# Kernel optimization log

Hardware: AMD Instinct MI355X
Metric: run time of the kernel (lower is better)

The kernel has to match this reference:

```python
import jax, jax.numpy as jnp
import numpy as np

HEAD_DIM = 64

def setup_inputs() -> dict:
    key = jax.random.key(0)
    k1, k2, k3, k4, k5 = jax.random.split(key, 5)
    T, B, E = 2048, 4, 1024
    KD = 64  # kdim
    x = jax.random.normal(k1, (T, B, E), dtype=jnp.float32)
    in_proj_weight = jax.random.normal(k2, (3 * KD, HEAD_DIM), dtype=jnp.float32) * (1.0 / np.sqrt(HEAD_DIM))
    in_proj_bias = jnp.zeros((3 * KD,), dtype=jnp.float32)
    out_w = jax.random.normal(k4, (HEAD_DIM, KD), dtype=jnp.float32) * (1.0 / np.sqrt(KD))
    out_b = jnp.zeros((HEAD_DIM,), dtype=jnp.float32)
    return {"x": x, "in_proj_weight": in_proj_weight, "in_proj_bias": in_proj_bias,
            "out_w": out_w, "out_b": out_b}

def reference(x, in_proj_weight, in_proj_bias, out_w, out_b):
    # x: [T, B, E] with E = H * HEAD_DIM (qkv_same self-attention path)
    T, B, E = x.shape
    H = E // HEAD_DIM
    KD = in_proj_weight.shape[0] // 3
    scaling = HEAD_DIM ** (-0.5)
    # reshape splits embed dim into heads: [T, B*H, 64]
    xh = x.reshape(T, B * H, HEAD_DIM)
    # fused in-projection: [T, B*H, 3*KD], then chunk into q/k/v
    qkv = xh @ in_proj_weight.T + in_proj_bias
    q, k, v = jnp.split(qkv, 3, axis=-1)          # each [T, B*H, KD]
    q = q * scaling
    q = q.transpose(1, 0, 2)                      # [B*H, T, KD]
    k = k.transpose(1, 0, 2)
    v = v.transpose(1, 0, 2)
    scores = jnp.einsum('btd,bsd->bts', q, k)     # [B*H, T, T]
    w = jax.nn.softmax(scores, axis=-1)
    attn = jnp.einsum('bts,bsd->btd', w, v)       # [B*H, T, KD]
    attn = attn.transpose(1, 0, 2).reshape(T, B, H, KD)
    out = attn @ out_w.T + out_b                  # [T, B, H, HEAD_DIM]
    out = out.reshape(T, B, H * HEAD_DIM)         # [T, B, E]
    # averaged attention weights over heads: [B, T, T]
    avg_w = w.reshape(B, H, T, T).sum(axis=1) / H
    return out, avg_w
```

## Files before the change

### kernel.cpp

```cpp
#include <hip/hip_runtime.h>
#include <hip/hip_bf16.h>

#define T_DIM 2048
#define B_DIM 4
#define E_DIM 1024

typedef __bf16 bf16_t;
typedef bf16_t bf16x8 __attribute__((ext_vector_type(8)));
typedef float f32x4 __attribute__((ext_vector_type(4)));
typedef float f32x16 __attribute__((ext_vector_type(16)));

union frag_u { uint4 u; bf16x8 b; };

constexpr float SCALEQ = 0.18033688011112042f;

__device__ __forceinline__ f32x16 mfma32(bf16x8 a, bf16x8 b, f32x16 c) {
  return __builtin_amdgcn_mfma_f32_32x32x16_bf16(a, b, c, 0, 0, 0);
}
__device__ __forceinline__ unsigned packbf(float a, float b) {
  union { bf16_t h[2]; unsigned u; } r;
  r.h[0] = (bf16_t)a; r.h[1] = (bf16_t)b; return r.u;
}
__device__ __forceinline__ void pl32swap(unsigned &x, unsigned &y) {
  asm volatile("v_permlane32_swap_b32 %0, %1" : "+v"(x), "+v"(y));
}
__device__ __forceinline__ void gload16(const void* g, void* l) {
  __builtin_amdgcn_global_load_lds((const __attribute__((address_space(1))) void*)g,
                                   (__attribute__((address_space(3))) void*)l, 16, 0, 0);
}
__device__ __forceinline__ bf16x8 ldc(const char* base, int chunk, int row) {
  frag_u f; f.u = *(const uint4*)(base + chunk * 1024 + row * 16); return f.b;
}
__device__ __forceinline__ float ex2(float x) { return __builtin_amdgcn_exp2f(x); }

#define VMCNT2 do { asm volatile("s_waitcnt vmcnt(2)" ::: "memory"); \
                    __builtin_amdgcn_sched_barrier(0); } while (0)
#define VMCNT0 do { asm volatile("s_waitcnt vmcnt(0)" ::: "memory"); \
                    __builtin_amdgcn_sched_barrier(0); } while (0)
#define LGKM0  do { asm volatile("s_waitcnt lgkmcnt(0)" ::: "memory"); \
                    __builtin_amdgcn_sched_barrier(0); } while (0)

template <int O>
__device__ __forceinline__ uint4 mkfrag(const f32x16& A) {
  unsigned X = packbf(A[O + 0], A[O + 1]);
  unsigned Z = packbf(A[O + 2], A[O + 3]);
  unsigned Y = packbf(A[O + 4], A[O + 5]);
  unsigned W = packbf(A[O + 6], A[O + 7]);
  pl32swap(X, Y); pl32swap(Z, W);
  return (uint4){X, Z, Y, W};
}

__global__ __launch_bounds__(256) void qkv_kernel(
    const float* __restrict__ x, const float* __restrict__ W,
    const float* __restrict__ bias,
    bf16_t* __restrict__ Qc, bf16_t* __restrict__ Kc, bf16_t* __restrict__ Vc) {
  __shared__ __align__(16) char xlds[16384];
  __shared__ __align__(16) char wlds[24576];
  __shared__ float bs[192];
  const int tid = threadIdx.x;
  const int bh = blockIdx.x >> 4;
  const int tt = blockIdx.x & 15;
  const int b = bh >> 4, h = bh & 15;
  const int t0 = tt * 128;
  const int wid = tid >> 6, lane = tid & 63;
  const int lq = lane & 31, hi = lane >> 5;

  for (int i = tid; i < 1024; i += 256) {
    int t = i >> 3, oct = i & 7;
    const float* src = x + ((size_t)(t0 + t) * B_DIM + b) * E_DIM + h * 64 + oct * 8;
    float4 f0 = *(const float4*)src;
    float4 f1 = *(const float4*)(src + 4);
    uint4 u;
    u.x = packbf(f0.x, f0.y); u.y = packbf(f0.z, f0.w);
    u.z = packbf(f1.x, f1.y); u.w = packbf(f1.z, f1.w);
    *(uint4*)(xlds + oct * 2048 + t * 16) = u;
  }
  for (int i = tid; i < 1536; i += 256) {
    int r = i >> 3, oct = i & 7;
    const float* src = W + r * 64 + oct * 8;
    float4 f0 = *(const float4*)src;
    float4 f1 = *(const float4*)(src + 4);
    uint4 u;
    u.x = packbf(f0.x, f0.y); u.y = packbf(f0.z, f0.w);
    u.z = packbf(f1.x, f1.y); u.w = packbf(f1.z, f1.w);
    *(uint4*)(wlds + oct * 3072 + r * 16) = u;
  }
  if (tid < 192) bs[tid] = bias[tid];
  __syncthreads();

  frag_u bx[4];
  #pragma unroll
  for (int s = 0; s < 4; ++s)
    bx[s].u = *(const uint4*)(xlds + (s * 2 + hi) * 2048 + (wid * 32 + lq) * 16);

  f32x16 acc[6];
  #pragma unroll
  for (int mt = 0; mt < 6; ++mt)
    #pragma unroll
    for (int r = 0; r < 16; ++r) acc[mt][r] = 0.f;

  #pragma unroll
  for (int mt = 0; mt < 6; ++mt) {
    #pragma unroll
    for (int s = 0; s < 4; ++s) {
      frag_u aw;
      aw.u = *(const uint4*)(wlds + (s * 2 + hi) * 3072 + (mt * 32 + lq) * 16);
      acc[mt] = mfma32(aw.b, bx[s].b, acc[mt]);
    }
  }

  const size_t tb = ((size_t)bh * 32 + (t0 >> 6) + (wid >> 1)) * 4096;
  const int trow = (wid & 1) * 32 + lq;

  #pragma unroll
  for (int mt = 0; mt < 6; ++mt) {
    #pragma unroll
    for (int g = 0; g < 4; ++g) {
      int rbase = mt * 32 + 8 * g + 4 * hi;
      float4 bq = *(const float4*)&bs[rbase];
      float v0 = acc[mt][4 * g + 0] + bq.x;
      float v1 = acc[mt][4 * g + 1] + bq.y;
      float v2 = acc[mt][4 * g + 2] + bq.z;
      float v3 = acc[mt][4 * g + 3] + bq.w;
      if (mt < 2) {
        union { ushort4 us; unsigned u2[2]; } pk;
        pk.u2[0] = packbf(v0 * SCALEQ, v1 * SCALEQ);
        pk.u2[1] = packbf(v2 * SCALEQ, v3 * SCALEQ);
        int d0 = rbase;
        *(ushort4*)(Qc + tb + (d0 >> 3) * 512 + trow * 8 + (d0 & 7)) = pk.us;
      } else if (mt < 4) {
        union { ushort4 us; unsigned u2[2]; } pk;
        pk.u2[0] = packbf(v0, v1);
        pk.u2[1] = packbf(v2, v3);
        int d0 = rbase - 64;
        *(ushort4*)(Kc + tb + (d0 >> 3) * 512 + trow * 8 + (d0 & 7)) = pk.us;
      } else {
        int d0 = rbase - 128;
        bf16_t* vdst = Vc + tb + (trow >> 3) * 512 + (trow & 7);
        vdst[(size_t)(d0 + 0) * 8] = (bf16_t)v0;
        vdst[(size_t)(d0 + 1) * 8] = (bf16_t)v1;
        vdst[(size_t)(d0 + 2) * 8] = (bf16_t)v2;
        vdst[(size_t)(d0 + 3) * 8] = (bf16_t)v3;
      }
    }
  }
}

__global__ __launch_bounds__(512, 2) void flash_kernel(
    const bf16_t* __restrict__ Qc, const bf16_t* __restrict__ Kc,
    const bf16_t* __restrict__ Vc,
    const float* __restrict__ Wo, const float* __restrict__ bo,
    float* __restrict__ out, float* __restrict__ Lv) {
  __shared__ __align__(16) char lds[32768];
  __shared__ __align__(16) char wlds[8192];
  const int tid = threadIdx.x;
  const int bid = ((blockIdx.x & 7) << 6) | (blockIdx.x >> 3);
  const int bh = bid >> 3, qb = bid & 7;
  const int b = bh >> 4, h = bh & 15;
  const int wid = tid >> 6, lane = tid & 63;
  const int lq = lane & 31, hi = lane >> 5;
  const int qw = qb * 256 + wid * 32;

  {
    const float* src = Wo + (tid >> 3) * 64 + (tid & 7) * 8;
    float4 f0 = *(const float4*)src;
    float4 f1 = *(const float4*)(src + 4);
    uint4 u;
    u.x = packbf(f0.x, f0.y); u.y = packbf(f0.z, f0.w);
    u.z = packbf(f1.x, f1.y); u.w = packbf(f1.z, f1.w);
    *(uint4*)(wlds + (tid & 7) * 1024 + (tid >> 3) * 16) = u;
  }

  const bf16_t* qtb = Qc + ((size_t)bh * 32 + (qw >> 6)) * 4096;
  const int qrow = qw & 63;
  frag_u qf[4];
  #pragma unroll
  for (int s = 0; s < 4; ++s)
    qf[s].u = *(const uint4*)(qtb + (s * 2 + hi) * 512 + (qrow + lq) * 8);

  f32x16 zc;
  #pragma unroll
  for (int i = 0; i < 16; ++i) zc[i] = 0.f;

  f32x16 o0, o1;
  #pragma unroll
  for (int i = 0; i < 16; ++i) { o0[i] = 0.f; o1[i] = 0.f; }
  float lacc = 0.f;

  const bf16_t* kbh = Kc + (size_t)bh * 131072;
  const bf16_t* vbh = Vc + (size_t)bh * 131072;
  auto stage = [&](int buf, int t) {
    char* kd = lds + buf * 16384;
    const bf16_t* kt = kbh + (size_t)t * 4096 + wid * 512 + lane * 8;
    const bf16_t* vt = vbh + (size_t)t * 4096 + wid * 512 + lane * 8;
    gload16(kt, kd + wid * 1024);
    gload16(vt, kd + 8192 + wid * 1024);
  };

  stage(0, 0); stage(1, 1);
  __syncthreads();

  for (int t = 0; t < 32; ++t) {
    const char* kl = lds + (t & 1) * 16384;
    const char* vl = kl + 8192;

    bf16x8 k0[4], k1[4];
    #pragma unroll
    for (int s = 0; s < 4; ++s) {
      k0[s] = ldc(kl, s * 2 + hi, lq);
      k1[s] = ldc(kl, s * 2 + hi, 32 + lq);
    }
    f32x16 a0, a1;
    __builtin_amdgcn_s_setprio(1);
    a0 = mfma32(k0[0], qf[0].b, zc);
    a1 = mfma32(k1[0], qf[0].b, zc);
    #pragma unroll
    for (int s = 1; s < 4; ++s) {
      a0 = mfma32(k0[s], qf[s].b, a0);
      a1 = mfma32(k1[s], qf[s].b, a1);
    }
    __builtin_amdgcn_s_setprio(0);

    bf16x8 v0[4], v1[4];
    #pragma unroll
    for (int ks = 0; ks < 4; ++ks) {
      v0[ks] = ldc(vl, ks * 2 + hi, lq);
      v1[ks] = ldc(vl, ks * 2 + hi, 32 + lq);
    }
    LGKM0;
    __builtin_amdgcn_s_barrier();
    if (t + 2 < 32) stage(t & 1, t + 2);

    float s0 = 0.f, s1 = 0.f;
    #pragma unroll
    for (int i = 0; i < 16; ++i) {
      a0[i] = ex2(a0[i]); s0 += a0[i];
      a1[i] = ex2(a1[i]); s1 += a1[i];
    }
    lacc += s0 + s1;

    frag_u p0, p1, p2, p3;
    p0.u = mkfrag<0>(a0); p1.u = mkfrag<8>(a0);
    p2.u = mkfrag<0>(a1); p3.u = mkfrag<8>(a1);

    __builtin_amdgcn_s_setprio(1);
    o0 = mfma32(v0[0], p0.b, o0); o1 = mfma32(v1[0], p0.b, o1);
    o0 = mfma32(v0[1], p1.b, o0); o1 = mfma32(v1[1], p1.b, o1);
    o0 = mfma32(v0[2], p2.b, o0); o1 = mfma32(v1[2], p2.b, o1);
    o0 = mfma32(v0[3], p3.b, o0); o1 = mfma32(v1[3], p3.b, o1);
    __builtin_amdgcn_s_setprio(0);

    if (t < 30) { VMCNT2; } else { VMCNT0; }
    __builtin_amdgcn_s_barrier();
  }

  float lt = lacc + __shfl_xor(lacc, 32);
  float inv = 1.f / lt;
  #pragma unroll
  for (int i = 0; i < 16; ++i) { o0[i] *= inv; o1[i] *= inv; }

  frag_u fo[4];
  fo[0].u = mkfrag<0>(o0); fo[1].u = mkfrag<8>(o0);
  fo[2].u = mkfrag<0>(o1); fo[3].u = mkfrag<8>(o1);

  f32x16 c0, c1;
  {
    frag_u w0, w1;
    w0.u = *(const uint4*)(wlds + (0 * 2 + hi) * 1024 + lq * 16);
    w1.u = *(const uint4*)(wlds + (0 * 2 + hi) * 1024 + (32 + lq) * 16);
    c0 = mfma32(fo[0].b, w0.b, zc);
    c1 = mfma32(fo[0].b, w1.b, zc);
    #pragma unroll
    for (int s = 1; s < 4; ++s) {
      w0.u = *(const uint4*)(wlds + (s * 2 + hi) * 1024 + lq * 16);
      w1.u = *(const uint4*)(wlds + (s * 2 + hi) * 1024 + (32 + lq) * 16);
      c0 = mfma32(fo[s].b, w0.b, c0);
      c1 = mfma32(fo[s].b, w1.b, c1);
    }
  }
  float bo0 = bo[lq], bo1 = bo[32 + lq];
  #pragma unroll
  for (int r = 0; r < 16; ++r) {
    int tr = qw + (r & 3) + 8 * (r >> 2) + 4 * hi;
    out[((size_t)tr * B_DIM + b) * E_DIM + h * 64 + lq]      = c0[r] + bo0;
    out[((size_t)tr * B_DIM + b) * E_DIM + h * 64 + 32 + lq] = c1[r] + bo1;
  }
  if (lane < 32)
    Lv[(size_t)bh * T_DIM + qw + lq] = lt;
}

__global__ __launch_bounds__(512, 2) void avgw_kernel(
    const bf16_t* __restrict__ Qc, const bf16_t* __restrict__ Kc,
    const float* __restrict__ Lv, float* __restrict__ avgw) {
  __shared__ __align__(16) char qlds[2][16384];
  __shared__ __align__(16) char klds[2][16384];
  __shared__ float lw[16][128];
  const int tid = threadIdx.x;
  const int bid = ((blockIdx.x & 7) << 7) | (blockIdx.x >> 3);
  const int b = bid >> 8, tq = (bid >> 4) & 15, sq = bid & 15;
  const int t0 = tq * 128, s0 = sq * 128;
  const int wid = tid >> 6, lane = tid & 63;
  const int lq = lane & 31, hi = lane >> 5;
  const int wr = wid >> 2, wc = wid & 3;

  for (int i = tid; i < 2048; i += 512) {
    int h = i >> 7, tt = i & 127;
    size_t idx = ((size_t)(b * 16 + h)) * T_DIM + t0 + tt;
    lw[h][tt] = 1.0f / (16.0f * Lv[idx]);
  }

  auto stage = [&](int buf, int h) {
    int bh = b * 16 + h;
    const bf16_t* qt = Qc + ((size_t)bh * 32 + (t0 >> 6)) * 4096;
    const bf16_t* kt = Kc + ((size_t)bh * 32 + (s0 >> 6)) * 4096;
    #pragma unroll
    for (int j = 0; j < 2; ++j) {
      gload16(qt + wid * 1024 + j * 512 + lane * 8, qlds[buf] + wid * 2048 + j * 1024);
      gload16(kt + wid * 1024 + j * 512 + lane * 8, klds[buf] + wid * 2048 + j * 1024);
    }
  };

  f32x16 zc;
  #pragma unroll
  for (int r = 0; r < 16; ++r) zc[r] = 0.f;

  f32x16 sacc[2];
  #pragma unroll
  for (int i = 0; i < 2; ++i)
    #pragma unroll
    for (int r = 0; r < 16; ++r) sacc[i][r] = 0.f;

  stage(0, 0);
  __syncthreads();

  for (int h = 0; h < 16; ++h) {
    if (h < 15) stage((h + 1) & 1, h + 1);
    const char* qb = qlds[h & 1];
    const char* kb = klds[h & 1];

    frag_u aq[2][4], ak[4];
    #pragma unroll
    for (int s = 0; s < 4; ++s) {
      int rk = wc * 32 + lq;
      ak[s].u = *(const uint4*)(kb + (rk >> 6) * 8192 + (s * 2 + hi) * 1024 + (rk & 63) * 16);
      #pragma unroll
      for (int i = 0; i < 2; ++i) {
        int rq = wr * 64 + i * 32 + lq;
        aq[i][s].u = *(const uint4*)(qb + (rq >> 6) * 8192 + (s * 2 + hi) * 1024 + (rq & 63) * 16);
      }
    }

    #pragma unroll
    for (int i = 0; i < 2; ++i) {
      __builtin_amdgcn_s_setprio(1);
      f32x16 c = mfma32(aq[i][0].b, ak[0].b, zc);
      #pragma unroll
      for (int s = 1; s < 4; ++s) c = mfma32(aq[i][s].b, ak[s].b, c);
      __builtin_amdgcn_s_setprio(0);
      #pragma unroll
      for (int g = 0; g < 4; ++g) {
        f32x4 l4 = *(const f32x4*)&lw[h][wr * 64 + i * 32 + 8 * g + 4 * hi];
        #pragma unroll
        for (int e = 0; e < 4; ++e)
          sacc[i][4 * g + e] += ex2(c[4 * g + e]) * l4[e];
      }
    }
    __syncthreads();
  }

  #pragma unroll
  for (int i = 0; i < 2; ++i)
    #pragma unroll
    for (int r = 0; r < 16; ++r) {
      int trow = t0 + wr * 64 + i * 32 + (r & 3) + ((r >> 2) << 3) + (hi << 2);
      int scol = s0 + wc * 32 + lq;
      avgw[((size_t)b * T_DIM + trow) * T_DIM + scol] = sacc[i][r];
    }
}

extern "C" void kernel_launch(void* const* d_in, const int* in_sizes, int n_in,
                              void* d_out, int out_size, void* d_ws, size_t ws_size,
                              hipStream_t stream) {
  const float* x    = (const float*)d_in[0];
  const float* W    = (const float*)d_in[1];
  const float* bias = (const float*)d_in[2];
  const float* Wo   = (const float*)d_in[3];
  const float* bo   = (const float*)d_in[4];
  float* out  = (float*)d_out;
  float* avgw = out + (size_t)T_DIM * B_DIM * E_DIM;

  char* ws = (char*)d_ws;
  bf16_t* Qc = (bf16_t*)(ws);
  bf16_t* Kc = (bf16_t*)(ws + (16u << 20));
  bf16_t* Vc = (bf16_t*)(ws + (32u << 20));
  float*  Lv = (float*)(ws + (48u << 20));

  qkv_kernel<<<dim3(1024), dim3(256), 0, stream>>>(x, W, bias, Qc, Kc, Vc);
  flash_kernel<<<dim3(512), dim3(512), 0, stream>>>(Qc, Kc, Vc, Wo, bo, out, Lv);
  avgw_kernel<<<dim3(1024), dim3(512), 0, stream>>>(Qc, Kc, Lv, avgw);
}
```

Before: 175.7 us.

## Halve flash block to 4 waves with two ping-ponged 32-row query tiles per wave

The flash kernel now runs 256 threads per block, and each wave owns 64 query rows split into two 32-row sub-tiles (A and B). Their QK^T MFMAs, exp2/softmax and PV MFMAs are staggered so vector work on one sub-tile overlaps matrix work on the other, and the next tile's QK for A is issued early. Each K/V tile is staged with twice as many loads per thread, and the wait scheme changes accordingly. The goal is to hide softmax latency and halve per-block K/V LDS reads per query, at the cost of more accumulator registers and fewer waves per CU.

```diff
diff --git a/kernel.cpp b/kernel.cpp
--- a/kernel.cpp
+++ b/kernel.cpp
@@ -33,11 +33,13 @@
 }
 __device__ __forceinline__ float ex2(float x) { return __builtin_amdgcn_exp2f(x); }
 
-#define VMCNT2 do { asm volatile("s_waitcnt vmcnt(2)" ::: "memory"); \
+#define VMCNT4 do { asm volatile("s_waitcnt vmcnt(4)" ::: "memory"); \
                     __builtin_amdgcn_sched_barrier(0); } while (0)
 #define VMCNT0 do { asm volatile("s_waitcnt vmcnt(0)" ::: "memory"); \
                     __builtin_amdgcn_sched_barrier(0); } while (0)
 #define LGKM0  do { asm volatile("s_waitcnt lgkmcnt(0)" ::: "memory"); \
+                    __builtin_amdgcn_sched_barrier(0); } while (0)
+#define SBAR   do { __builtin_amdgcn_s_barrier(); \
                     __builtin_amdgcn_sched_barrier(0); } while (0)
 
 template <int O>
@@ -146,7 +148,7 @@
   }
 }
 
-__global__ __launch_bounds__(512, 2) void flash_kernel(
+__global__ __launch_bounds__(256, 2) void flash_kernel(
     const bf16_t* __restrict__ Qc, const bf16_t* __restrict__ Kc,
     const bf16_t* __restrict__ Vc,
     const float* __restrict__ Wo, const float* __restrict__ bo,
@@ -159,67 +161,93 @@
   const int b = bh >> 4, h = bh & 15;
   const int wid = tid >> 6, lane = tid & 63;
   const int lq = lane & 31, hi = lane >> 5;
-  const int qw = qb * 256 + wid * 32;
-
-  {
-    const float* src = Wo + (tid >> 3) * 64 + (tid & 7) * 8;
+  const int qw = qb * 256 + wid * 64;
+
+  for (int i = tid; i < 512; i += 256) {
+    int d = i >> 3, oct = i & 7;
+    const float* src = Wo + d * 64 + oct * 8;
     float4 f0 = *(const float4*)src;
     float4 f1 = *(const float4*)(src + 4);
     uint4 u;
     u.x = packbf(f0.x, f0.y); u.y = packbf(f0.z, f0.w);
     u.z = packbf(f1.x, f1.y); u.w = packbf(f1.z, f1.w);
-    *(uint4*)(wlds + (tid & 7) * 1024 + (tid >> 3) * 16) = u;
+    *(uint4*)(wlds + oct * 1024 + d * 16) = u;
   }
 
   const bf16_t* qtb = Qc + ((size_t)bh * 32 + (qw >> 6)) * 4096;
-  const int qrow = qw & 63;
-  frag_u qf[4];
-  #pragma unroll
-  for (int s = 0; s < 4; ++s)
-    qf[s].u = *(const uint4*)(qtb + (s * 2 + hi) * 512 + (qrow + lq) * 8);
+  frag_u qfA[4], qfB[4];
+  #pragma unroll
+  for (int s = 0; s < 4; ++s) {
+    qfA[s].u = *(const uint4*)(qtb + (s * 2 + hi) * 512 + lq * 8);
+    qfB[s].u = *(const uint4*)(qtb + (s * 2 + hi) * 512 + (32 + lq) * 8);
+  }
 
   f32x16 zc;
   #pragma unroll
   for (int i = 0; i < 16; ++i) zc[i] = 0.f;
 
-  f32x16 o0, o1;
-  #pragma unroll
-  for (int i = 0; i < 16; ++i) { o0[i] = 0.f; o1[i] = 0.f; }
-  float lacc = 0.f;
+  f32x16 oA0, oA1, oB0, oB1;
+  #pragma unroll
+  for (int i = 0; i < 16; ++i) { oA0[i] = 0.f; oA1[i] = 0.f; oB0[i] = 0.f; oB1[i] = 0.f; }
+  float lAacc = 0.f, lBacc = 0.f;
 
   const bf16_t* kbh = Kc + (size_t)bh * 131072;
   const bf16_t* vbh = Vc + (size_t)bh * 131072;
   auto stage = [&](int buf, int t) {
-    char* kd = lds + buf * 16384;
+    char* kl_ = lds + buf * 16384 + wid * 1024;
+    char* vl_ = kl_ + 8192;
     const bf16_t* kt = kbh + (size_t)t * 4096 + wid * 512 + lane * 8;
     const bf16_t* vt = vbh + (size_t)t * 4096 + wid * 512 + lane * 8;
-    gload16(kt, kd + wid * 1024);
-    gload16(vt, kd + 8192 + wid * 1024);
+    gload16(kt, kl_); gload16(kt + 2048, kl_ + 4096);
+    gload16(vt, vl_); gload16(vt + 2048, vl_ + 4096);
   };
 
   stage(0, 0); stage(1, 1);
-  __syncthreads();
-
-  for (int t = 0; t < 32; ++t) {
-    const char* kl = lds + (t & 1) * 16384;
-    const char* vl = kl + 8192;
-
-    bf16x8 k0[4], k1[4];
+  VMCNT4; LGKM0;
+  SBAR;
+
+  bf16x8 k0[4], k1[4];
+  {
+    const char* kl = lds;
     #pragma unroll
     for (int s = 0; s < 4; ++s) {
       k0[s] = ldc(kl, s * 2 + hi, lq);
       k1[s] = ldc(kl, s * 2 + hi, 32 + lq);
     }
-    f32x16 a0, a1;
+  }
+  f32x16 aA0, aA1;
+  aA0 = mfma32(k0[0], qfA[0].b, zc);
+  aA1 = mfma32(k1[0], qfA[0].b, zc);
+  #pragma unroll
+  for (int s = 1; s < 4; ++s) {
+    aA0 = mfma32(k0[s], qfA[s].b, aA0);
+    aA1 = mfma32(k1[s], qfA[s].b, aA1);
+  }
+
+  for (int t = 0; t < 32; ++t) {
+    const char* cb = lds + (t & 1) * 16384;
+    const char* vl = cb + 8192;
+
+    f32x16 aB0, aB1;
     __builtin_amdgcn_s_setprio(1);
-    a0 = mfma32(k0[0], qf[0].b, zc);
-    a1 = mfma32(k1[0], qf[0].b, zc);
+    aB0 = mfma32(k0[0], qfB[0].b, zc);
+    aB1 = mfma32(k1[0], qfB[0].b, zc);
     #pragma unroll
     for (int s = 1; s < 4; ++s) {
-      a0 = mfma32(k0[s], qf[s].b, a0);
-      a1 = mfma32(k1[s], qf[s].b, a1);
+      aB0 = mfma32(k0[s], qfB[s].b, aB0);
+      aB1 = mfma32(k1[s], qfB[s].b, aB1);
     }
     __builtin_amdgcn_s_setprio(0);
+    float sA = 0.f;
+    #pragma unroll
+    for (int i = 0; i < 16; ++i) {
+      aA0[i] = ex2(aA0[i]); sA += aA0[i];
+      aA1[i] = ex2(aA1[i]); sA += aA1[i];
+    }
+    lAacc += sA;
+    frag_u pA0, pA1, pA2, pA3;
+    pA0.u = mkfrag<0>(aA0); pA1.u = mkfrag<8>(aA0);
+    pA2.u = mkfrag<0>(aA1); pA3.u = mkfrag<8>(aA1);
 
     bf16x8 v0[4], v1[4];
     #pragma unroll
@@ -227,66 +255,92 @@
       v0[ks] = ldc(vl, ks * 2 + hi, lq);
       v1[ks] = ldc(vl, ks * 2 + hi, 32 + lq);
     }
-    LGKM0;
-    __builtin_amdgcn_s_barrier();
+
+    __builtin_amdgcn_s_setprio(1);
+    oA0 = mfma32(v0[0], pA0.b, oA0); oA1 = mfma32(v1[0], pA0.b, oA1);
+    oA0 = mfma32(v0[1], pA1.b, oA0); oA1 = mfma32(v1[1], pA1.b, oA1);
+    oA0 = mfma32(v0[2], pA2.b, oA0); oA1 = mfma32(v1[2], pA2.b, oA1);
+    oA0 = mfma32(v0[3], pA3.b, oA0); oA1 = mfma32(v1[3], pA3.b, oA1);
+    __builtin_amdgcn_s_setprio(0);
+    float sB = 0.f;
+    #pragma unroll
+    for (int i = 0; i < 16; ++i) {
+      aB0[i] = ex2(aB0[i]); sB += aB0[i];
+      aB1[i] = ex2(aB1[i]); sB += aB1[i];
+    }
+    lBacc += sB;
+    frag_u pB0, pB1, pB2, pB3;
+    pB0.u = mkfrag<0>(aB0); pB1.u = mkfrag<8>(aB0);
+    pB2.u = mkfrag<0>(aB1); pB3.u = mkfrag<8>(aB1);
+
+    VMCNT0;
+    SBAR;
     if (t + 2 < 32) stage(t & 1, t + 2);
 
-    float s0 = 0.f, s1 = 0.f;
-    #pragma unroll
-    for (int i = 0; i < 16; ++i) {
-      a0[i] = ex2(a0[i]); s0 += a0[i];
-      a1[i] = ex2(a1[i]); s1 += a1[i];
-    }
-    lacc += s0 + s1;
-
-    frag_u p0, p1, p2, p3;
-    p0.u = mkfrag<0>(a0); p1.u = mkfrag<8>(a0);
-    p2.u = mkfrag<0>(a1); p3.u = mkfrag<8>(a1);
-
     __builtin_amdgcn_s_setprio(1);
-    o0 = mfma32(v0[0], p0.b, o0); o1 = mfma32(v1[0], p0.b, o1);
-    o0 = mfma32(v0[1], p1.b, o0); o1 = mfma32(v1[1], p1.b, o1);
-    o0 = mfma32(v0[2], p2.b, o0); o1 = mfma32(v1[2], p2.b, o1);
-    o0 = mfma32(v0[3], p3.b, o0); o1 = mfma32(v1[3], p3.b, o1);
+    oB0 = mfma32(v0[0], pB0.b, oB0); oB1 = mfma32(v1[0], pB0.b, oB1);
+    oB0 = mfma32(v0[1], pB1.b, oB0); oB1 = mfma32(v1[1], pB1.b, oB1);
+    oB0 = mfma32(v0[2], pB2.b, oB0); oB1 = mfma32(v1[2], pB2.b, oB1);
+    oB0 = mfma32(v0[3], pB3.b, oB0); oB1 = mfma32(v1[3], pB3.b, oB1);
     __builtin_amdgcn_s_setprio(0);
-
-    if (t < 30) { VMCNT2; } else { VMCNT0; }
-    __builtin_amdgcn_s_barrier();
-  }
-
-  float lt = lacc + __shfl_xor(lacc, 32);
-  float inv = 1.f / lt;
-  #pragma unroll
-  for (int i = 0; i < 16; ++i) { o0[i] *= inv; o1[i] *= inv; }
-
-  frag_u fo[4];
-  fo[0].u = mkfrag<0>(o0); fo[1].u = mkfrag<8>(o0);
-  fo[2].u = mkfrag<0>(o1); fo[3].u = mkfrag<8>(o1);
-
-  f32x16 c0, c1;
-  {
+    if (t < 31) {
+      const char* kn = lds + ((t + 1) & 1) * 16384;
+      #pragma unroll
+      for (int s = 0; s < 4; ++s) {
+        k0[s] = ldc(kn, s * 2 + hi, lq);
+        k1[s] = ldc(kn, s * 2 + hi, 32 + lq);
+      }
+      __builtin_amdgcn_s_setprio(1);
+      aA0 = mfma32(k0[0], qfA[0].b, zc);
+      aA1 = mfma32(k1[0], qfA[0].b, zc);
+      #pragma unroll
+      for (int s = 1; s < 4; ++s) {
+        aA0 = mfma32(k0[s], qfA[s].b, aA0);
+        aA1 = mfma32(k1[s], qfA[s].b, aA1);
+      }
+      __builtin_amdgcn_s_setprio(0);
+    }
+  }
+
+  float ltA = lAacc + __shfl_xor(lAacc, 32);
+  float ltB = lBacc + __shfl_xor(lBacc, 32);
+  float iA = 1.f / ltA, iB = 1.f / ltB;
+  #pragma unroll
+  for (int i = 0; i < 16; ++i) { oA0[i] *= iA; oA1[i] *= iA; oB0[i] *= iB; oB1[i] *= iB; }
+
+  frag_u fA[4], fB[4];
+  fA[0].u = mkfrag<0>(oA0); fA[1].u = mkfrag<8>(oA0);
+  fA[2].u = mkfrag<0>(oA1); fA[3].u = mkfrag<8>(oA1);
+  fB[0].u = mkfrag<0>(oB0); fB[1].u = mkfrag<8>(oB0);
+  fB[2].u = mkfrag<0>(oB1); fB[3].u = mkfrag<8>(oB1);
+
+  f32x16 cA0, cA1, cB0, cB1;
+  #pragma unroll
+  for (int i = 0; i < 16; ++i) { cA0[i] = 0.f; cA1[i] = 0.f; cB0[i] = 0.f; cB1[i] = 0.f; }
+  #pragma unroll
+  for (int s = 0; s < 4; ++s) {
     frag_u w0, w1;
-    w0.u = *(const uint4*)(wlds + (0 * 2 + hi) * 1024 + lq * 16);
-    w1.u = *(const uint4*)(wlds + (0 * 2 + hi) * 1024 + (32 + lq) * 16);
-    c0 = mfma32(fo[0].b, w0.b, zc);
-    c1 = mfma32(fo[0].b, w1.b, zc);
-    #pragma unroll
-    for (int s = 1; s < 4; ++s) {
-      w0.u = *(const uint4*)(wlds + (s * 2 + hi) * 1024 + lq * 16);
-      w1.u = *(const uint4*)(wlds + (s * 2 + hi) * 1024 + (32 + lq) * 16);
-      c0 = mfma32(fo[s].b, w0.b, c0);
-      c1 = mfma32(fo[s].b, w1.b, c1);
-    }
+    w0.u = *(const uint4*)(wlds + (s * 2 + hi) * 1024 + lq * 16);
+    w1.u = *(const uint4*)(wlds + (s * 2 + hi) * 1024 + (32 + lq) * 16);
+    cA0 = mfma32(fA[s].b, w0.b, cA0);
+    cA1 = mfma32(fA[s].b, w1.b, cA1);
+    cB0 = mfma32(fB[s].b, w0.b, cB0);
+    cB1 = mfma32(fB[s].b, w1.b, cB1);
   }
   float bo0 = bo[lq], bo1 = bo[32 + lq];
   #pragma unroll
   for (int r = 0; r < 16; ++r) {
-    int tr = qw + (r & 3) + 8 * (r >> 2) + 4 * hi;
-    out[((size_t)tr * B_DIM + b) * E_DIM + h * 64 + lq]      = c0[r] + bo0;
-    out[((size_t)tr * B_DIM + b) * E_DIM + h * 64 + 32 + lq] = c1[r] + bo1;
-  }
-  if (lane < 32)
-    Lv[(size_t)bh * T_DIM + qw + lq] = lt;
+    int trA = qw + (r & 3) + 8 * (r >> 2) + 4 * hi;
+    int trB = trA + 32;
+    out[((size_t)trA * B_DIM + b) * E_DIM + h * 64 + lq]      = cA0[r] + bo0;
+    out[((size_t)trA * B_DIM + b) * E_DIM + h * 64 + 32 + lq] = cA1[r] + bo1;
+    out[((size_t)trB * B_DIM + b) * E_DIM + h * 64 + lq]      = cB0[r] + bo0;
+    out[((size_t)trB * B_DIM + b) * E_DIM + h * 64 + 32 + lq] = cB1[r] + bo1;
+  }
+  if (lane < 32) {
+    Lv[(size_t)bh * T_DIM + qw + lq] = ltA;
+    Lv[(size_t)bh * T_DIM + qw + 32 + lq] = ltB;
+  }
 }
 
 __global__ __launch_bounds__(512, 2) void avgw_kernel(
@@ -396,6 +450,6 @@
   float*  Lv = (float*)(ws + (48u << 20));
 
   qkv_kernel<<<dim3(1024), dim3(256), 0, stream>>>(x, W, bias, Qc, Kc, Vc);
-  flash_kernel<<<dim3(512), dim3(512), 0, stream>>>(Qc, Kc, Vc, Wo, bo, out, Lv);
+  flash_kernel<<<dim3(512), dim3(256), 0, stream>>>(Qc, Kc, Vc, Wo, bo, out, Lv);
   avgw_kernel<<<dim3(1024), dim3(512), 0, stream>>>(Qc, Kc, Lv, avgw);
 }
```

Result: no change. 174.3 us (-0.8%).
